# Kernel tuning notes

Measured on AMD Instinct MI355X. Metric: run time of the kernel, lower is better.

## Reference

```python
import jax, jax.numpy as jnp
import numpy as np

B = 1024        # number of graphs in batch
NNODES = 64     # nodes per graph
NODE = 4        # node feature size
EDGEF = 2       # edge feature size
HID = 32        # hidden_dim
NFACT = 3       # num_factories
NE = 1024       # edges per graph (self.edges list length)


def setup_inputs() -> dict:
    key = jax.random.key(0)
    ks = jax.random.split(key, 12)
    rng = np.random.default_rng(1)
    # per-graph edge list (self.edges in the torch module)
    edges = rng.integers(0, NNODES, size=(NE, 2))
    edges_src = jnp.asarray(edges[:, 0], dtype=jnp.int32)   # [NE]
    edges_dst = jnp.asarray(edges[:, 1], dtype=jnp.int32)   # [NE]
    # batched edge_index for EdgeConv: same per-graph edges offset by b*NNODES
    offs = np.arange(B, dtype=np.int64)[:, None] * NNODES   # [B,1]
    ei_src = (edges[:, 0][None, :] + offs).reshape(-1)
    ei_dst = (edges[:, 1][None, :] + offs).reshape(-1)
    edge_index = jnp.asarray(np.stack([ei_src, ei_dst], 0), dtype=jnp.int32)  # [2, B*NE]

    N = B * NNODES
    E = B * NE
    x = jax.random.normal(ks[0], (N, NODE), dtype=jnp.float32)
    edge_attr = jax.random.normal(ks[1], (E, EDGEF), dtype=jnp.float32)
    action = jax.random.uniform(ks[2], (B, NE + NFACT), dtype=jnp.float32)

    s = 0.1
    W1 = jax.random.normal(ks[3], (2 * NODE + EDGEF, HID), dtype=jnp.float32) * s
    b1 = jnp.zeros((HID,), jnp.float32)
    W2 = jax.random.normal(ks[4], (HID, HID), dtype=jnp.float32) * s
    b2 = jnp.zeros((HID,), jnp.float32)
    D = (NODE + HID) * 2 + 1  # 73
    Wl = jax.random.normal(ks[5], (D, HID), dtype=jnp.float32) * s
    bl = jnp.zeros((HID,), jnp.float32)
    Wv = jax.random.normal(ks[6], (HID, 1), dtype=jnp.float32) * s
    bv = jnp.zeros((1,), jnp.float32)

    return {"x": x, "edge_index": edge_index, "edge_attr": edge_attr,
            "action": action, "edges_src": edges_src, "edges_dst": edges_dst,
            "W1": W1, "b1": b1, "W2": W2, "b2": b2,
            "Wl": Wl, "bl": bl, "Wv": Wv, "bv": bv}


def reference(x, edge_index, edge_attr, action, edges_src, edges_dst,
              W1, b1, W2, b2, Wl, bl, Wv, bv):
    N = x.shape[0]
    src = edge_index[0]  # flow='target_to_source': x_i = x[src], aggregate at src
    dst = edge_index[1]
    # EdgeConv message: MLP(cat[x_i, x_j, edge_attr])
    tmp = jnp.concatenate([x[src], x[dst], edge_attr], axis=1)  # [E, 10]
    msg = jax.nn.relu(tmp @ W1 + b1) @ W2 + b2                  # [E, HID]
    x_pp = jax.ops.segment_sum(msg, src, num_segments=N)        # scatter-add
    # concat node feats with conv output, split into graphs
    h = jnp.concatenate([x, x_pp], axis=1).reshape(B, NNODES, NODE + HID)  # [B,NN,36]
    # gather per-edge endpoint features
    ef = jnp.concatenate([h[:, edges_src], h[:, edges_dst]], axis=2)       # [B,NE,72]
    # factory features: last NFACT nodes duplicated
    pf = jnp.concatenate([h[:, -NFACT:], h[:, -NFACT:]], axis=-1)          # [B,NF,72]
    feats = jnp.concatenate([ef, pf], axis=1)                               # [B,NE+NF,72]
    concat = jnp.concatenate([feats, action[..., None]], axis=-1)           # [B,NE+NF,73]
    hidden = jax.nn.relu(concat @ Wl + bl)                                  # [B,NE+NF,HID]
    v = hidden @ Wv + bv                                                    # [B,NE+NF,1]
    return jnp.sum(v, axis=1).squeeze(-1)                                   # [B]
```

## Files before the change

### kernel.cpp

```cpp
#include <hip/hip_runtime.h>

#define NNODES 64
#define HID 32
#define NFACT 3
#define NE 1024
#define NROWS (NE + NFACT)
#define TPB 256
#define STR 36
#define MAXTILES 128

#define WS_DEG  64
#define WS_TN   128
#define WS_PE   256

typedef short bf16x8 __attribute__((ext_vector_type(8)));
typedef float f32x4  __attribute__((ext_vector_type(4)));

__device__ __forceinline__ unsigned pack_bf2(float lo, float hi) {
    unsigned ul = __builtin_bit_cast(unsigned, lo);
    unsigned uh = __builtin_bit_cast(unsigned, hi);
    ul += 0x7fffu + ((ul >> 16) & 1u);
    uh += 0x7fffu + ((uh >> 16) & 1u);
    return (ul >> 16) | (uh & 0xffff0000u);
}
__device__ __forceinline__ short f2bf(float f) {
    unsigned u = __builtin_bit_cast(unsigned, f);
    u += 0x7fffu + ((u >> 16) & 1u);
    return (short)(u >> 16);
}
__device__ __forceinline__ float4 fma4(float a, float4 w, float4 c) {
    c.x = fmaf(a, w.x, c.x); c.y = fmaf(a, w.y, c.y);
    c.z = fmaf(a, w.z, c.z); c.w = fmaf(a, w.w, c.w);
    return c;
}

__global__ __launch_bounds__(TPB) void build_csr(const int* __restrict__ es,
                                                 const int* __restrict__ ed,
                                                 int* __restrict__ ws) {
    __shared__ int sdeg[NNODES], soff[NNODES], scnt[NNODES];
    const int tid = threadIdx.x;
    if (tid < NNODES) { sdeg[tid] = 0; scnt[tid] = 0; }
    if (tid < MAXTILES) ws[WS_TN + tid] = 0;
#pragma unroll 1
    for (int i = tid; i < MAXTILES * 16; i += TPB) ws[WS_PE + i] = 0xFFFF;
    __syncthreads();
#pragma unroll 1
    for (int e = tid; e < NE; e += TPB) atomicAdd(&sdeg[es[e]], 1);
    __syncthreads();
    if (tid == 0) {
        int run = 0;
#pragma unroll 1
        for (int n = 0; n < NNODES; n++) { soff[n] = run; run += (sdeg[n] + 15) >> 4; }
        ws[0] = run;
    }
    __syncthreads();
    if (tid < NNODES) {
        ws[WS_DEG + tid] = sdeg[tid];
        const int base = soff[tid], cnt = (sdeg[tid] + 15) >> 4;
#pragma unroll 1
        for (int j = 0; j < cnt; j++) ws[WS_TN + base + j] = tid;
    }
    __syncthreads();
#pragma unroll 1
    for (int e = tid; e < NE; e += TPB) {
        const int n = es[e];
        const int idx = atomicAdd(&scnt[n], 1);
        ws[WS_PE + soff[n] * 16 + idx] = e | (ed[e] << 16);
    }
}

__global__ __launch_bounds__(TPB, 4) void critic_fused(
    const float* __restrict__ x,
    const float* __restrict__ edge_attr,
    const float* __restrict__ action,
    const int*   __restrict__ es,
    const int*   __restrict__ ed,
    const float* __restrict__ W1,
    const float* __restrict__ b1,
    const float* __restrict__ W2,
    const float* __restrict__ b2,
    const float* __restrict__ Wl,
    const float* __restrict__ bl,
    const float* __restrict__ Wv,
    const float* __restrict__ bv,
    const int*   __restrict__ csr,
    float* __restrict__ out)
{
    const int b    = blockIdx.x;
    const int tid  = threadIdx.x;
    const int lane = tid & 63;
    const int wv   = tid >> 6;

    __shared__ float4 xs4[NNODES];
    __shared__ float  xpp[NNODES * STR];
    __shared__ float  qp0[NNODES * STR];
    __shared__ float  qp1[NNODES * STR];
    __shared__ float  W1s[10 * HID];
    __shared__ float  Wls[73 * HID];
    __shared__ float  b1s[HID], bls[HID], b2s[HID];
    __shared__ float  wred[TPB / 64];

    if (tid < NNODES) xs4[tid] = ((const float4*)x)[b * NNODES + tid];
    {
        float4*       W1s4 = (float4*)W1s;
        const float4* W1g  = (const float4*)W1;
        if (tid < 80) W1s4[tid] = W1g[tid];
        float4*       Wls4 = (float4*)Wls;
        const float4* Wlg  = (const float4*)Wl;
#pragma unroll 1
        for (int i = tid; i < 73 * HID / 4; i += TPB) Wls4[i] = Wlg[i];
        if (tid < HID) { b1s[tid] = b1[tid]; bls[tid] = bl[tid]; b2s[tid] = b2[tid]; }
    }
#pragma unroll 1
    for (int i = tid; i < NNODES * STR; i += TPB) xpp[i] = 0.0f;
    __syncthreads();

    const int n  = tid & 63;
    const int k0 = (tid >> 6) * 8;

    {
        const float4 xv = xs4[n];
        const float4* b1v = (const float4*)&b1s[k0];
        float4 q1a = b1v[0], q1b = b1v[1];
        float4 q2a = make_float4(0.f, 0.f, 0.f, 0.f), q2b = q2a;
#pragma unroll 1
        for (int i = 0; i < 4; i++) {
            const float xi = (i == 0) ? xv.x : (i == 1) ? xv.y : (i == 2) ? xv.z : xv.w;
            const float4* wa = (const float4*)&W1s[i * HID + k0];
            const float4* wb = (const float4*)&W1s[(4 + i) * HID + k0];
            q1a = fma4(xi, wa[0], q1a); q1b = fma4(xi, wa[1], q1b);
            q2a = fma4(xi, wb[0], q2a); q2b = fma4(xi, wb[1], q2b);
        }
        float4* q1w = (float4*)&qp0[n * STR + k0];
        float4* q2w = (float4*)&qp1[n * STR + k0];
        q1w[0] = q1a; q1w[1] = q1b;
        q2w[0] = q2a; q2w[1] = q2b;
    }
    __syncthreads();

    {
        const float2* ea2 = (const float2*)edge_attr + (size_t)b * NE;
        const int quad = lane >> 4;
        const int m16  = lane & 15;
        const int kh   = quad * 8;
        const int NW   = TPB / 64;

        const float4* w8p = (const float4*)&W1s[8 * HID + kh];
        const float4* w9p = (const float4*)&W1s[9 * HID + kh];
        const float4 w8a = w8p[0], w8b = w8p[1];
        const float4 w9a = w9p[0], w9b = w9p[1];

        bf16x8 bf0, bf1;
#pragma unroll
        for (int j = 0; j < 8; j++) {
            bf0[j] = f2bf(W2[(kh + j) * HID + m16]);
            bf1[j] = f2bf(W2[(kh + j) * HID + 16 + m16]);
        }

        const int  ntiles = csr[0];
        const int* tn  = csr + WS_TN;
        const int* pep = csr + WS_PE;

#pragma unroll 1
        for (int t = wv; t < ntiles; t += NW) {
            const int raw  = pep[t * 16 + m16];
            const int node = tn[t];
            const int e    = raw & 0xFFFF;
            const bool pad = (e == 0xFFFF);
            const int d0   = raw >> 16;
            const float2 ea = ea2[pad ? 0 : e];

            const float4* Ap = (const float4*)&qp0[node * STR + kh];
            const float4  A0 = Ap[0], A1 = Ap[1];
            const float4* Gp = (const float4*)&qp1[d0 * STR + kh];
            const float4  G0 = Gp[0], G1 = Gp[1];

            const float h0 = fmaxf(A0.x + G0.x + ea.x * w8a.x + ea.y * w9a.x, 0.f);
            const float h1 = fmaxf(A0.y + G0.y + ea.x * w8a.y + ea.y * w9a.y, 0.f);
            const float h2 = fmaxf(A0.z + G0.z + ea.x * w8a.z + ea.y * w9a.z, 0.f);
            const float h3 = fmaxf(A0.w + G0.w + ea.x * w8a.w + ea.y * w9a.w, 0.f);
            const float h4 = fmaxf(A1.x + G1.x + ea.x * w8b.x + ea.y * w9b.x, 0.f);
            const float h5 = fmaxf(A1.y + G1.y + ea.x * w8b.y + ea.y * w9b.y, 0.f);
            const float h6 = fmaxf(A1.z + G1.z + ea.x * w8b.z + ea.y * w9b.z, 0.f);
            const float h7 = fmaxf(A1.w + G1.w + ea.x * w8b.w + ea.y * w9b.w, 0.f);

            uint4 packed;
            packed.x = pad ? 0u : pack_bf2(h0, h1);
            packed.y = pad ? 0u : pack_bf2(h2, h3);
            packed.z = pad ? 0u : pack_bf2(h4, h5);
            packed.w = pad ? 0u : pack_bf2(h6, h7);
            const bf16x8 af = __builtin_bit_cast(bf16x8, packed);

            f32x4 c0 = {0.f, 0.f, 0.f, 0.f};
            f32x4 c1 = {0.f, 0.f, 0.f, 0.f};
            c0 = __builtin_amdgcn_mfma_f32_16x16x32_bf16(af, bf0, c0, 0, 0, 0);
            c1 = __builtin_amdgcn_mfma_f32_16x16x32_bf16(af, bf1, c1, 0, 0, 0);

            float s0 = c0[0] + c0[1] + c0[2] + c0[3];
            float s1 = c1[0] + c1[1] + c1[2] + c1[3];
            s0 += __shfl_xor(s0, 16); s0 += __shfl_xor(s0, 32);
            s1 += __shfl_xor(s1, 16); s1 += __shfl_xor(s1, 32);
            if (lane < 32)
                atomicAdd(&xpp[node * STR + lane], (lane < 16) ? s0 : s1);
        }
    }
    __syncthreads();

    {
        const float4 xv = xs4[n];
        const float dn = (float)csr[WS_DEG + n];
        const float4* blv = (const float4*)&bls[k0];
        float4 p1a = blv[0], p1b = blv[1];
        float4 p2a = make_float4(0.f, 0.f, 0.f, 0.f), p2b = p2a;
#pragma unroll 1
        for (int i = 0; i < 4; i++) {
            const float xi = (i == 0) ? xv.x : (i == 1) ? xv.y : (i == 2) ? xv.z : xv.w;
            const float4* wa = (const float4*)&Wls[i * HID + k0];
            const float4* wb = (const float4*)&Wls[(36 + i) * HID + k0];
            p1a = fma4(xi, wa[0], p1a); p1b = fma4(xi, wa[1], p1b);
            p2a = fma4(xi, wb[0], p2a); p2b = fma4(xi, wb[1], p2b);
        }
        const float4* xrv  = (const float4*)&xpp[n * STR];
        const float4* b2v4 = (const float4*)b2s;
#pragma unroll 1
        for (int q = 0; q < 8; q++) {
            float4 xq = xrv[q];
            const float4 bq = b2v4[q];
            xq.x = fmaf(dn, bq.x, xq.x); xq.y = fmaf(dn, bq.y, xq.y);
            xq.z = fmaf(dn, bq.z, xq.z); xq.w = fmaf(dn, bq.w, xq.w);
            const int j = q * 4;
#pragma unroll
            for (int u = 0; u < 4; u++) {
                const float xj = (u == 0) ? xq.x : (u == 1) ? xq.y : (u == 2) ? xq.z : xq.w;
                const float4* wa = (const float4*)&Wls[(4 + j + u) * HID + k0];
                const float4* wb = (const float4*)&Wls[(40 + j + u) * HID + k0];
                p1a = fma4(xj, wa[0], p1a); p1b = fma4(xj, wa[1], p1b);
                p2a = fma4(xj, wb[0], p2a); p2b = fma4(xj, wb[1], p2b);
            }
        }
        float4* p1w = (float4*)&qp0[n * STR + k0];
        float4* p2w = (float4*)&qp1[n * STR + k0];
        p1w[0] = p1a; p1w[1] = p1b;
        p2w[0] = p2a; p2w[1] = p2b;
    }
    __syncthreads();

    float vsum = 0.0f;
    {
        const float* actb = action + (size_t)b * NROWS;
        const float bvv = bv[0];
        const float* Wl72 = Wl + 72 * HID;
#pragma unroll 1
        for (int i = 0; i < 4; i++) {
            const int r = tid + i * TPB;
            const int na = es[r], nb = ed[r];
            const float a = actb[r];
            const float4* p1v = (const float4*)&qp0[na * STR];
            const float4* p2v = (const float4*)&qp1[nb * STR];
            float v0 = bvv, v1 = 0.0f;
#pragma unroll 1
            for (int q = 0; q < 8; q += 2) {
                const float4 pa0 = p1v[q],     pb0 = p2v[q];
                const float4 pa1 = p1v[q + 1], pb1 = p2v[q + 1];
                const int k = q * 4;
                v0 += fmaxf(pa0.x + pb0.x + a * Wl72[k+0], 0.f) * Wv[k+0];
                v1 += fmaxf(pa0.y + pb0.y + a * Wl72[k+1], 0.f) * Wv[k+1];
                v0 += fmaxf(pa0.z + pb0.z + a * Wl72[k+2], 0.f) * Wv[k+2];
                v1 += fmaxf(pa0.w + pb0.w + a * Wl72[k+3], 0.f) * Wv[k+3];
                v0 += fmaxf(pa1.x + pb1.x + a * Wl72[k+4], 0.f) * Wv[k+4];
                v1 += fmaxf(pa1.y + pb1.y + a * Wl72[k+5], 0.f) * Wv[k+5];
                v0 += fmaxf(pa1.z + pb1.z + a * Wl72[k+6], 0.f) * Wv[k+6];
                v1 += fmaxf(pa1.w + pb1.w + a * Wl72[k+7], 0.f) * Wv[k+7];
            }
            vsum += v0 + v1;
        }
        if (tid < NFACT) {
            const int r = NE + tid;
            const int na = NNODES - NFACT + tid;
            const float a = actb[r];
            const float4* p1v = (const float4*)&qp0[na * STR];
            const float4* p2v = (const float4*)&qp1[na * STR];
            float v = bvv;
#pragma unroll 1
            for (int q = 0; q < 8; q++) {
                const float4 pa = p1v[q], pb = p2v[q];
                const int k = q * 4;
                v += fmaxf(pa.x + pb.x + a * Wl72[k+0], 0.f) * Wv[k+0];
                v += fmaxf(pa.y + pb.y + a * Wl72[k+1], 0.f) * Wv[k+1];
                v += fmaxf(pa.z + pb.z + a * Wl72[k+2], 0.f) * Wv[k+2];
                v += fmaxf(pa.w + pb.w + a * Wl72[k+3], 0.f) * Wv[k+3];
            }
            vsum += v;
        }
    }

#pragma unroll
    for (int off = 32; off > 0; off >>= 1)
        vsum += __shfl_down(vsum, off, 64);
    if ((tid & 63) == 0) wred[tid >> 6] = vsum;
    __syncthreads();
    if (tid == 0) {
        float t = 0.0f;
#pragma unroll
        for (int w = 0; w < TPB / 64; w++) t += wred[w];
        out[b] = t;
    }
}

extern "C" void kernel_launch(void* const* d_in, const int* in_sizes, int n_in,
                              void* d_out, int out_size, void* d_ws, size_t ws_size,
                              hipStream_t stream) {
    const float* x         = (const float*)d_in[0];
    const float* edge_attr = (const float*)d_in[2];
    const float* action    = (const float*)d_in[3];
    const int*   es        = (const int*)d_in[4];
    const int*   ed        = (const int*)d_in[5];
    const float* W1        = (const float*)d_in[6];
    const float* b1        = (const float*)d_in[7];
    const float* W2        = (const float*)d_in[8];
    const float* b2        = (const float*)d_in[9];
    const float* Wl        = (const float*)d_in[10];
    const float* bl        = (const float*)d_in[11];
    const float* Wv        = (const float*)d_in[12];
    const float* bv        = (const float*)d_in[13];
    float* out = (float*)d_out;
    int*   ws  = (int*)d_ws;

    build_csr<<<dim3(1), dim3(TPB), 0, stream>>>(es, ed, ws);
    critic_fused<<<dim3(out_size), dim3(TPB), 0, stream>>>(
        x, edge_attr, action, es, ed, W1, b1, W2, b2, Wl, bl, Wv, bv, ws, out);
}
```

Before: 142.2 us.

## Compute node projection stage with bf16 MFMA and drop shared Wl staging

The per-node projection of the convolution output through Wl was a scalar FMA loop reading Wl from shared memory. It now packs the aggregated features into bf16 and runs four 16x16x32 MFMAs per wave, with the x-part and bias pre-seeded into the accumulators. The Wl, bl and b2 values each lane needs are held in registers, so the large Wl shared-memory copy goes away, and the launch bound rises to 5 blocks per CU. This lowers per-block LDS use and setup loads but adds register pressure and bf16 rounding to that stage.

```diff
diff --git a/kernel.cpp b/kernel.cpp
--- a/kernel.cpp
+++ b/kernel.cpp
@@ -69,7 +69,7 @@
     }
 }
 
-__global__ __launch_bounds__(TPB, 4) void critic_fused(
+__global__ __launch_bounds__(TPB, 5) void critic_fused(
     const float* __restrict__ x,
     const float* __restrict__ edge_attr,
     const float* __restrict__ action,
@@ -90,29 +90,46 @@
     const int tid  = threadIdx.x;
     const int lane = tid & 63;
     const int wv   = tid >> 6;
+    const int quad = lane >> 4;
+    const int m16  = lane & 15;
+    const int kh   = quad * 8;
 
     __shared__ float4 xs4[NNODES];
     __shared__ float  xpp[NNODES * STR];
     __shared__ float  qp0[NNODES * STR];
     __shared__ float  qp1[NNODES * STR];
     __shared__ float  W1s[10 * HID];
-    __shared__ float  Wls[73 * HID];
-    __shared__ float  b1s[HID], bls[HID], b2s[HID];
+    __shared__ float  b1s[HID];
     __shared__ float  wred[TPB / 64];
 
     if (tid < NNODES) xs4[tid] = ((const float4*)x)[b * NNODES + tid];
-    {
-        float4*       W1s4 = (float4*)W1s;
-        const float4* W1g  = (const float4*)W1;
-        if (tid < 80) W1s4[tid] = W1g[tid];
-        float4*       Wls4 = (float4*)Wls;
-        const float4* Wlg  = (const float4*)Wl;
-#pragma unroll 1
-        for (int i = tid; i < 73 * HID / 4; i += TPB) Wls4[i] = Wlg[i];
-        if (tid < HID) { b1s[tid] = b1[tid]; bls[tid] = bl[tid]; b2s[tid] = b2[tid]; }
-    }
+    if (tid < 80) ((float4*)W1s)[tid] = ((const float4*)W1)[tid];
+    if (tid < HID) b1s[tid] = b1[tid];
 #pragma unroll 1
     for (int i = tid; i < NNODES * STR; i += TPB) xpp[i] = 0.0f;
+
+    bf16x8 bP1a, bP1b, bP2a, bP2b;
+#pragma unroll
+    for (int j = 0; j < 8; j++) {
+        bP1a[j] = f2bf(Wl[(4 + kh + j) * HID + m16]);
+        bP1b[j] = f2bf(Wl[(4 + kh + j) * HID + 16 + m16]);
+        bP2a[j] = f2bf(Wl[(40 + kh + j) * HID + m16]);
+        bP2b[j] = f2bf(Wl[(40 + kh + j) * HID + 16 + m16]);
+    }
+    float wx1a[4], wx1b[4], wx2a[4], wx2b[4];
+#pragma unroll
+    for (int i = 0; i < 4; i++) {
+        wx1a[i] = Wl[i * HID + m16];
+        wx1b[i] = Wl[i * HID + 16 + m16];
+        wx2a[i] = Wl[(36 + i) * HID + m16];
+        wx2b[i] = Wl[(36 + i) * HID + 16 + m16];
+    }
+    const float blca = bl[m16], blcb = bl[16 + m16];
+    float b2k[8];
+#pragma unroll
+    for (int j = 0; j < 8; j++) b2k[j] = b2[kh + j];
+    const int   mrow = wv * 16 + m16;
+    const float dn   = (float)csr[WS_DEG + mrow];
     __syncthreads();
 
     const int n  = tid & 63;
@@ -140,10 +157,7 @@
 
     {
         const float2* ea2 = (const float2*)edge_attr + (size_t)b * NE;
-        const int quad = lane >> 4;
-        const int m16  = lane & 15;
-        const int kh   = quad * 8;
-        const int NW   = TPB / 64;
+        const int NW = TPB / 64;
 
         const float4* w8p = (const float4*)&W1s[8 * HID + kh];
         const float4* w9p = (const float4*)&W1s[9 * HID + kh];
@@ -207,41 +221,47 @@
     __syncthreads();
 
     {
-        const float4 xv = xs4[n];
-        const float dn = (float)csr[WS_DEG + n];
-        const float4* blv = (const float4*)&bls[k0];
-        float4 p1a = blv[0], p1b = blv[1];
-        float4 p2a = make_float4(0.f, 0.f, 0.f, 0.f), p2b = p2a;
-#pragma unroll 1
-        for (int i = 0; i < 4; i++) {
-            const float xi = (i == 0) ? xv.x : (i == 1) ? xv.y : (i == 2) ? xv.z : xv.w;
-            const float4* wa = (const float4*)&Wls[i * HID + k0];
-            const float4* wb = (const float4*)&Wls[(36 + i) * HID + k0];
-            p1a = fma4(xi, wa[0], p1a); p1b = fma4(xi, wa[1], p1b);
-            p2a = fma4(xi, wb[0], p2a); p2b = fma4(xi, wb[1], p2b);
-        }
-        const float4* xrv  = (const float4*)&xpp[n * STR];
-        const float4* b2v4 = (const float4*)b2s;
-#pragma unroll 1
-        for (int q = 0; q < 8; q++) {
-            float4 xq = xrv[q];
-            const float4 bq = b2v4[q];
-            xq.x = fmaf(dn, bq.x, xq.x); xq.y = fmaf(dn, bq.y, xq.y);
-            xq.z = fmaf(dn, bq.z, xq.z); xq.w = fmaf(dn, bq.w, xq.w);
-            const int j = q * 4;
-#pragma unroll
-            for (int u = 0; u < 4; u++) {
-                const float xj = (u == 0) ? xq.x : (u == 1) ? xq.y : (u == 2) ? xq.z : xq.w;
-                const float4* wa = (const float4*)&Wls[(4 + j + u) * HID + k0];
-                const float4* wb = (const float4*)&Wls[(40 + j + u) * HID + k0];
-                p1a = fma4(xj, wa[0], p1a); p1b = fma4(xj, wa[1], p1b);
-                p2a = fma4(xj, wb[0], p2a); p2b = fma4(xj, wb[1], p2b);
+        const float4* xr = (const float4*)&xpp[mrow * STR + kh];
+        float4 x0 = xr[0], x1 = xr[1];
+        x0.x = fmaf(dn, b2k[0], x0.x); x0.y = fmaf(dn, b2k[1], x0.y);
+        x0.z = fmaf(dn, b2k[2], x0.z); x0.w = fmaf(dn, b2k[3], x0.w);
+        x1.x = fmaf(dn, b2k[4], x1.x); x1.y = fmaf(dn, b2k[5], x1.y);
+        x1.z = fmaf(dn, b2k[6], x1.z); x1.w = fmaf(dn, b2k[7], x1.w);
+        uint4 packed;
+        packed.x = pack_bf2(x0.x, x0.y);
+        packed.y = pack_bf2(x0.z, x0.w);
+        packed.z = pack_bf2(x1.x, x1.y);
+        packed.w = pack_bf2(x1.z, x1.w);
+        const bf16x8 af = __builtin_bit_cast(bf16x8, packed);
+
+        f32x4 c1a, c1b, c2a, c2b;
+#pragma unroll
+        for (int r = 0; r < 4; r++) {
+            const float4 xv = xs4[wv * 16 + quad * 4 + r];
+            float a0 = blca, a1 = blcb, a2 = 0.f, a3 = 0.f;
+#pragma unroll
+            for (int i = 0; i < 4; i++) {
+                const float xi = (i == 0) ? xv.x : (i == 1) ? xv.y : (i == 2) ? xv.z : xv.w;
+                a0 = fmaf(xi, wx1a[i], a0);
+                a1 = fmaf(xi, wx1b[i], a1);
+                a2 = fmaf(xi, wx2a[i], a2);
+                a3 = fmaf(xi, wx2b[i], a3);
             }
-        }
-        float4* p1w = (float4*)&qp0[n * STR + k0];
-        float4* p2w = (float4*)&qp1[n * STR + k0];
-        p1w[0] = p1a; p1w[1] = p1b;
-        p2w[0] = p2a; p2w[1] = p2b;
+            c1a[r] = a0; c1b[r] = a1; c2a[r] = a2; c2b[r] = a3;
+        }
+        c1a = __builtin_amdgcn_mfma_f32_16x16x32_bf16(af, bP1a, c1a, 0, 0, 0);
+        c1b = __builtin_amdgcn_mfma_f32_16x16x32_bf16(af, bP1b, c1b, 0, 0, 0);
+        c2a = __builtin_amdgcn_mfma_f32_16x16x32_bf16(af, bP2a, c2a, 0, 0, 0);
+        c2b = __builtin_amdgcn_mfma_f32_16x16x32_bf16(af, bP2b, c2b, 0, 0, 0);
+
+#pragma unroll
+        for (int r = 0; r < 4; r++) {
+            const int row = wv * 16 + quad * 4 + r;
+            qp0[row * STR + m16]      = c1a[r];
+            qp0[row * STR + 16 + m16] = c1b[r];
+            qp1[row * STR + m16]      = c2a[r];
+            qp1[row * STR + 16 + m16] = c2b[r];
+        }
     }
     __syncthreads();
 
```

After: 148.6 us. 1.04x slower.
